# Kernel optimization log

Measured on AMD Instinct MI355X. Metric: run time of the kernel, lower is better.

## Reference

```python
import jax, jax.numpy as jnp
import numpy as np

B, S, HID = 1, 2048, 3072
NH, NKV, HD = 24, 8, 128
SCALING = 128.0 ** -0.5
SOFTCAP = 50.0
EPS = 1e-6
NEG = -1e9


def setup_inputs() -> dict:
    key = jax.random.key(0)
    ks = jax.random.split(key, 8)
    inv_freq = 1.0 / (10000.0 ** (jnp.arange(0, HD, 2, dtype=jnp.float32) / HD))
    pos = jnp.arange(S, dtype=jnp.float32)
    freqs = jnp.outer(pos, inv_freq)                      # [S, HD/2]
    emb = jnp.concatenate([freqs, freqs], axis=-1)        # [S, HD]
    cos = jnp.cos(emb)[None]                              # [B, S, HD]
    sin = jnp.sin(emb)[None]
    causal = jnp.tril(jnp.ones((S, S), dtype=bool))
    attention_mask = jnp.where(causal, 0.0, NEG).astype(jnp.float32)[None, None]  # [1,1,S,S]
    return {
        'hidden_states': jax.random.normal(ks[0], (B, S, HID), jnp.float32),
        'cos': cos,
        'sin': sin,
        'attention_mask': attention_mask,
        'wq': jax.random.normal(ks[1], (NH * HD, HID), jnp.float32) * 0.02,
        'wk': jax.random.normal(ks[2], (NKV * HD, HID), jnp.float32) * 0.02,
        'wv': jax.random.normal(ks[3], (NKV * HD, HID), jnp.float32) * 0.02,
        'wo': jax.random.normal(ks[4], (HID, NH * HD), jnp.float32) * 0.02,
        'q_norm_w': jnp.zeros((HD,), jnp.float32),
        'k_norm_w': jnp.zeros((HD,), jnp.float32),
    }


def _rms_norm(x, w, eps=EPS):
    xf = x.astype(jnp.float32)
    out = xf * jax.lax.rsqrt(jnp.mean(xf * xf, axis=-1, keepdims=True) + eps)
    return (out * (1.0 + w.astype(jnp.float32))).astype(x.dtype)


def _rotate_half(x):
    x1, x2 = jnp.split(x, 2, axis=-1)
    return jnp.concatenate([-x2, x1], axis=-1)


def reference(hidden_states, cos, sin, attention_mask, wq, wk, wv, wo, q_norm_w, k_norm_w):
    b, s, _ = hidden_states.shape
    q = jnp.einsum('bsd,ed->bse', hidden_states, wq).reshape(b, s, NH, HD).transpose(0, 2, 1, 3)
    k = jnp.einsum('bsd,ed->bse', hidden_states, wk).reshape(b, s, NKV, HD).transpose(0, 2, 1, 3)
    v = jnp.einsum('bsd,ed->bse', hidden_states, wv).reshape(b, s, NKV, HD).transpose(0, 2, 1, 3)
    q = _rms_norm(q, q_norm_w)
    k = _rms_norm(k, k_norm_w)
    c = cos[:, None]  # [B,1,S,HD]
    sn = sin[:, None]
    q = q * c + _rotate_half(q) * sn
    k = k * c + _rotate_half(k) * sn
    n_rep = NH // NKV
    k = jnp.repeat(k, n_rep, axis=1)  # [B,NH,S,HD]
    v = jnp.repeat(v, n_rep, axis=1)
    scores = jnp.einsum('bhqd,bhkd->bhqk', q, k) * SCALING
    scores = jnp.tanh(scores / SOFTCAP) * SOFTCAP
    scores = scores + attention_mask
    probs = jax.nn.softmax(scores.astype(jnp.float32), axis=-1).astype(q.dtype)
    out = jnp.einsum('bhqk,bhkd->bhqd', probs, v)
    out = out.transpose(0, 2, 1, 3).reshape(b, s, NH * HD)
    return jnp.einsum('bse,de->bsd', out, wo)
```

## Files before the change

kernel.cpp:

```cpp
#include <hip/hip_runtime.h>
#include <hip/hip_bf16.h>

#define S_LEN 2048
#define HIDV  3072
#define NHQ   24
#define NKVH  8
#define HDIM  128

typedef __bf16 bf16x8 __attribute__((ext_vector_type(8)));
typedef float  f32x4  __attribute__((ext_vector_type(4)));
typedef int    i32x4  __attribute__((ext_vector_type(4)));

__device__ __forceinline__ void gload_lds16(const void* g, void* l) {
    __builtin_amdgcn_global_load_lds((__attribute__((address_space(1))) void*)g,
                                     (__attribute__((address_space(3))) void*)l, 16, 0, 0);
}

__global__ void cast_all(const float* __restrict__ hs, const float* __restrict__ wq,
                         const float* __restrict__ wk, const float* __restrict__ wv,
                         const float* __restrict__ wo,
                         __hip_bfloat16* __restrict__ hsb, __hip_bfloat16* __restrict__ wf,
                         __hip_bfloat16* __restrict__ wob) {
    int c = blockIdx.x * blockDim.x + threadIdx.x;
    const float* src; __hip_bfloat16* dst; int off;
    if (c < 1572864)      { src = hs; dst = hsb;            off = c; }
    else if (c < 3932160) { src = wq; dst = wf;             off = c - 1572864; }
    else if (c < 4718592) { src = wk; dst = wf + 9437184;   off = c - 3932160; }
    else if (c < 5505024) { src = wv; dst = wf + 12582912;  off = c - 4718592; }
    else                  { src = wo; dst = wob;            off = c - 5505024; }
    float4 v = *(const float4*)(src + off * 4);
    union { __hip_bfloat16 h[4]; ushort4 u; } pk;
    pk.h[0] = __float2bfloat16(v.x);
    pk.h[1] = __float2bfloat16(v.y);
    pk.h[2] = __float2bfloat16(v.z);
    pk.h[3] = __float2bfloat16(v.w);
    *(ushort4*)(dst + off * 4) = pk.u;
}

template<int NF, int MODE>
__global__ __launch_bounds__(256) void gemm_tile(const __hip_bfloat16* __restrict__ A,
                                                 const __hip_bfloat16* __restrict__ B,
                                                 void* __restrict__ C0, void* __restrict__ C1,
                                                 void* __restrict__ C2)
{
    extern __shared__ __align__(16) char smem[];
    const int tid = threadIdx.x;
    const int w    = tid >> 6;
    const int lane = tid & 63;
    const int lr = lane & 15, lg = lane >> 4;
    const int wr = w >> 1, wc = w & 1;

    const int wg = ((int)blockIdx.x & 7) * 64 + ((int)blockIdx.x >> 3);
    const int bn = wg >> 4, bm = wg & 15;

    f32x4 zf = {0.f, 0.f, 0.f, 0.f};
    f32x4 acc[4][NF];
#pragma unroll
    for (int i = 0; i < 4; ++i)
#pragma unroll
        for (int j = 0; j < NF; ++j) acc[i][j] = zf;

    const char* Ab = (const char*)A + (size_t)(bm * 128) * 6144;
    const char* Bb = (const char*)B + (size_t)(bn * NF * 32) * 6144;
    const int NT = 48;

    int gaof[4], gbof[NF];
#pragma unroll
    for (int u_ = 0; u_ < 4; ++u_) {
        int u = tid + 256 * u_;
        int r_ = u >> 3, o_ = (u & 7) * 16;
        gaof[u_] = r_ * 6144 + (o_ ^ ((r_ & 7) << 4));
    }
#pragma unroll
    for (int u_ = 0; u_ < NF; ++u_) {
        int u = tid + 256 * u_;
        int r_ = u >> 3, o_ = (u & 7) * 16;
        gbof[u_] = r_ * 6144 + (o_ ^ ((r_ & 7) << 4));
    }

#define GT_STAGE(BUF, t) do {                                                       \
        const char* Abk_ = Ab + ((t) << 7);                                         \
        const char* Bbk_ = Bb + ((t) << 7);                                         \
        _Pragma("unroll")                                                           \
        for (int u_ = 0; u_ < 4; ++u_)                                              \
            gload_lds16(Abk_ + gaof[u_], smem + (BUF) * 16384 + tid * 16 + u_ * 4096); \
        _Pragma("unroll")                                                           \
        for (int u_ = 0; u_ < NF; ++u_)                                             \
            gload_lds16(Bbk_ + gbof[u_], smem + 32768 + (BUF) * (NF * 4096) + tid * 16 + u_ * 4096); \
    } while (0)

#define GT_COMPUTE(BUF) do {                                                        \
        bf16x8 af[4][2], bfr[NF][2];                                                \
        _Pragma("unroll")                                                           \
        for (int i = 0; i < 4; ++i) {                                               \
            int row = wr * 64 + i * 16 + lr;                                        \
            _Pragma("unroll")                                                       \
            for (int kk = 0; kk < 2; ++kk) {                                        \
                int cb = (kk * 64 + lg * 16) ^ ((row & 7) << 4);                    \
                af[i][kk] = *(const bf16x8*)(smem + (BUF) * 16384 + row * 128 + cb); \
            }                                                                       \
        }                                                                           \
        _Pragma("unroll")                                                           \
        for (int j = 0; j < NF; ++j) {                                              \
            int row = (wc * NF + j) * 16 + lr;                                      \
            _Pragma("unroll")                                                       \
            for (int kk = 0; kk < 2; ++kk) {                                        \
                int cb = (kk * 64 + lg * 16) ^ ((row & 7) << 4);                    \
                bfr[j][kk] = *(const bf16x8*)(smem + 32768 + (BUF) * (NF * 4096) + row * 128 + cb); \
            }                                                                       \
        }                                                                           \
        _Pragma("unroll")                                                           \
        for (int mi = 0; mi < 4; ++mi)                                              \
            _Pragma("unroll")                                                       \
            for (int ni = 0; ni < NF; ++ni)                                         \
                _Pragma("unroll")                                                   \
                for (int kk = 0; kk < 2; ++kk)                                      \
                    acc[mi][ni] = __builtin_amdgcn_mfma_f32_16x16x32_bf16(af[mi][kk], bfr[ni][kk], acc[mi][ni], 0, 0, 0); \
    } while (0)

    GT_STAGE(0, 0);
    __syncthreads();

    for (int t = 0; t < NT; t += 2) {
        GT_STAGE(1, t + 1);
        GT_COMPUTE(0);
        __syncthreads();
        if (t + 2 < NT) GT_STAGE(0, t + 2);
        GT_COMPUTE(1);
        __syncthreads();
    }
#undef GT_STAGE
#undef GT_COMPUTE

#pragma unroll
    for (int mi = 0; mi < 4; ++mi)
#pragma unroll
        for (int ni = 0; ni < NF; ++ni) {
            int row0 = bm * 128 + wr * 64 + mi * 16 + lg * 4;
            int col  = bn * NF * 32 + wc * NF * 16 + ni * 16 + lr;
            f32x4 v = acc[mi][ni];
            if (MODE == 0) {
#pragma unroll
                for (int j = 0; j < 4; ++j)
                    ((float*)C0)[(size_t)(row0 + j) * 3072 + col] = v[j];
            } else {
                if (col < 3072) {
#pragma unroll
                    for (int j = 0; j < 4; ++j)
                        ((__hip_bfloat16*)C0)[(size_t)(row0 + j) * 3072 + col] = __float2bfloat16(v[j]);
                } else if (col < 4096) {
#pragma unroll
                    for (int j = 0; j < 4; ++j)
                        ((__hip_bfloat16*)C1)[(size_t)(row0 + j) * 1024 + (col - 3072)] = __float2bfloat16(v[j]);
                } else {
                    union { __hip_bfloat16 h[4]; ushort4 u; } pk;
#pragma unroll
                    for (int j = 0; j < 4; ++j) pk.h[j] = __float2bfloat16(v[j]);
                    *(ushort4*)((__hip_bfloat16*)C2 + (size_t)(col - 4096) * 2048 + row0) = pk.u;
                }
            }
        }
}

__global__ void norm_rope_fused(const __hip_bfloat16* __restrict__ qpre,
                                const __hip_bfloat16* __restrict__ kpre,
                                __hip_bfloat16* __restrict__ qb, __hip_bfloat16* __restrict__ kb,
                                const float* __restrict__ qnw, const float* __restrict__ knw,
                                const float* __restrict__ cosp, const float* __restrict__ sinp)
{
    int gw = blockIdx.x * 4 + (threadIdx.x >> 6);
    int lane = threadIdx.x & 63;
    const __hip_bfloat16* row;
    const float* nw;
    __hip_bfloat16* outp;
    int s;
    if (gw < 49152) {
        s = gw / 24; int h = gw - s * 24;
        row  = qpre + (size_t)s * 3072 + h * HDIM;
        outp = qb   + (size_t)s * 3072 + h * HDIM;
        nw = qnw;
    } else {
        int g = gw - 49152;
        s = g >> 3; int h = g & 7;
        row  = kpre + (size_t)s * 1024 + h * HDIM;
        outp = kb + (size_t)h * 262144 + (size_t)s * 128;
        nw = knw;
    }
    float x1 = __bfloat162float(row[lane]), x2 = __bfloat162float(row[lane + 64]);
    float ss = x1 * x1 + x2 * x2;
#pragma unroll
    for (int xm = 1; xm < 64; xm <<= 1) ss += __shfl_xor(ss, xm, 64);
    float rs = rsqrtf(ss * (1.f / 128.f) + 1e-6f);
    float n1 = x1 * rs * (1.f + nw[lane]);
    float n2 = x2 * rs * (1.f + nw[lane + 64]);
    float c1 = cosp[s * HDIM + lane], c2 = cosp[s * HDIM + lane + 64];
    float s1 = sinp[s * HDIM + lane], s2 = sinp[s * HDIM + lane + 64];
    outp[lane]      = __float2bfloat16(n1 * c1 - n2 * s1);
    outp[lane + 64] = __float2bfloat16(n2 * c2 + n1 * s2);
}

__global__ __launch_bounds__(384) void attn_kernel(
    const __hip_bfloat16* __restrict__ Q,
    const __hip_bfloat16* __restrict__ Kc,
    const __hip_bfloat16* __restrict__ Vt,
    __hip_bfloat16* __restrict__ O)
{
    extern __shared__ __align__(16) char smem[];
    const int bid = blockIdx.x;
    const int kh = bid & 7;
    const int pb = bid >> 3;
    const int tid = threadIdx.x;
    const int w = tid >> 6;
    const int lane = tid & 63;
    const int lr = lane & 15, lg = lane >> 4;
    const int h = kh * 3 + (w >> 1);
    const int strip = w & 1;

    const char* kg = (const char*)(Kc + (size_t)kh * S_LEN * HDIM);
    const char* vg = (const char*)(Vt + (size_t)kh * HDIM * S_LEN);
    __hip_bfloat16* pw = (__hip_bfloat16*)(smem + 65536 + w * 2304);

    int ksrc[4], vsrc[4];
#pragma unroll
    for (int i_ = 0; i_ < 4; ++i_) {
        int base_ = (tid + 256 * i_) * 16;
        int kr_ = base_ >> 8, kc_ = base_ & 255;
        ksrc[i_] = kr_ * 256 + (kc_ ^ ((kr_ & 7) << 4));
        int vr_ = base_ >> 7, vc_ = base_ & 127;
        vsrc[i_] = vr_ * 4096 + (vc_ ^ ((vr_ & 7) << 4));
    }

#define ATT_STAGE(b, j0s) do {                                                      \
        if (tid < 256) {                                                            \
            const char* kgs_ = kg + (size_t)(j0s) * 256;                            \
            const char* vgs_ = vg + (size_t)(j0s) * 2;                              \
            _Pragma("unroll")                                                       \
            for (int i_ = 0; i_ < 4; ++i_) {                                        \
                gload_lds16(kgs_ + ksrc[i_], smem + (b) * 16384 + tid * 16 + i_ * 4096); \
                gload_lds16(vgs_ + vsrc[i_], smem + 32768 + (b) * 16384 + tid * 16 + i_ * 4096); \
            } } } while (0)

    for (int half = 0; half < 2; ++half) {
        const int hb = half ? (63 - pb) : pb;
        const int q0 = hb * 32;
        const int qrow = q0 + strip * 16;
        const int jtmax = (q0 + 31) >> 6;

        bf16x8 aq[4];
        {
            const __hip_bfloat16* qp = Q + (size_t)(qrow + lr) * HIDV + h * HDIM + lg * 8;
#pragma unroll
            for (int ks = 0; ks < 4; ++ks) aq[ks] = *(const bf16x8*)(qp + ks * 32);
        }

        f32x4 zf = {0.f, 0.f, 0.f, 0.f};
        f32x4 oacc[8];
#pragma unroll
        for (int i = 0; i < 8; ++i) oacc[i] = zf;
        float lacc[4] = {0.f, 0.f, 0.f, 0.f};

        ATT_STAGE(0, 0);
        __syncthreads();

        int buf = 0;
        for (int jt = 0; jt <= jtmax; ++jt) {
            if (jt < jtmax) ATT_STAGE(buf ^ 1, (jt + 1) * 64);

            const int j0 = jt * 64;
            const char* Kb = smem + buf * 16384;
            const char* Vb = smem + 32768 + buf * 16384;

            f32x4 sf[4];
#pragma unroll
            for (int nf = 0; nf < 4; ++nf) {
                sf[nf] = zf;
                int row = nf * 16 + lr;
#pragma unroll
                for (int ks = 0; ks < 4; ++ks) {
                    int boff = (row * 256 + ks * 64 + lg * 16) ^ ((row & 7) << 4);
                    bf16x8 bk = *(const bf16x8*)(Kb + boff);
                    sf[nf] = __builtin_amdgcn_mfma_f32_16x16x32_bf16(aq[ks], bk, sf[nf], 0, 0, 0);
                }
            }

            const bool diag = (jt == jtmax);
#pragma unroll
            for (int nf = 0; nf < 4; ++nf) {
                int jpos = j0 + nf * 16 + lr;
#pragma unroll
                for (int r = 0; r < 4; ++r) {
                    float sv = sf[nf][r];
                    float x2   = sv * sv * 3.125e-06f;
                    float poly = fmaf(x2, fmaf(x2, 0.13333333f, -0.33333333f), 1.0f);
                    float t    = sv * 0.08838834764831845f * poly;
                    float p    = __expf(t - 30.f);
                    if (diag && jpos > (qrow + lg * 4 + r)) p = 0.f;
                    lacc[r] += p;
                    pw[(lg * 4 + r) * 72 + nf * 16 + lr] = __float2bfloat16(p);
                }
            }

#pragma unroll
            for (int ks2 = 0; ks2 < 2; ++ks2) {
                bf16x8 ap = *(const bf16x8*)((const char*)pw + lr * 144 + ks2 * 64 + lg * 16);
#pragma unroll
                for (int df = 0; df < 8; ++df) {
                    int row = df * 16 + lr;
                    int boff = (row * 128 + ks2 * 64 + lg * 16) ^ ((row & 7) << 4);
                    bf16x8 bv = *(const bf16x8*)(Vb + boff);
                    oacc[df] = __builtin_amdgcn_mfma_f32_16x16x32_bf16(ap, bv, oacc[df], 0, 0, 0);
                }
            }
            __syncthreads();
            buf ^= 1;
        }

#pragma unroll
        for (int r = 0; r < 4; ++r) {
            float t = lacc[r];
#pragma unroll
            for (int xm = 1; xm < 16; xm <<= 1) t += __shfl_xor(t, xm, 64);
            float inv = __builtin_amdgcn_rcpf(t);
            size_t rowoff = (size_t)(qrow + lg * 4 + r) * HIDV + h * HDIM;
#pragma unroll
            for (int df = 0; df < 8; ++df)
                O[rowoff + df * 16 + lr] = __float2bfloat16(oacc[df][r] * inv);
        }
    }
#undef ATT_STAGE
}

extern "C" void kernel_launch(void* const* d_in, const int* in_sizes, int n_in,
                              void* d_out, int out_size, void* d_ws, size_t ws_size,
                              hipStream_t stream) {
    const float* hs   = (const float*)d_in[0];
    const float* cosp = (const float*)d_in[1];
    const float* sinp = (const float*)d_in[2];
    const float* wq  = (const float*)d_in[4];
    const float* wk  = (const float*)d_in[5];
    const float* wv  = (const float*)d_in[6];
    const float* wo  = (const float*)d_in[7];
    const float* qnw = (const float*)d_in[8];
    const float* knw = (const float*)d_in[9];
    float* out = (float*)d_out;

    char* ws = (char*)d_ws;
    __hip_bfloat16* hsb  = (__hip_bfloat16*)(ws + 0);
    __hip_bfloat16* wf   = (__hip_bfloat16*)(ws + 12582912);
    __hip_bfloat16* wob  = (__hip_bfloat16*)(ws + 44040192);
    __hip_bfloat16* qpre = (__hip_bfloat16*)(ws + 62914560);
    __hip_bfloat16* kpre = (__hip_bfloat16*)(ws + 75497472);
    __hip_bfloat16* qb   = (__hip_bfloat16*)(ws + 79691776);
    __hip_bfloat16* kb   = (__hip_bfloat16*)(ws + 92274688);
    __hip_bfloat16* vbt  = (__hip_bfloat16*)(ws + 96468992);
    __hip_bfloat16* ob   = (__hip_bfloat16*)(ws + 100663296);

    cast_all<<<30720, 256, 0, stream>>>(hs, wq, wk, wv, wo, hsb, wf, wob);

    gemm_tile<5, 1><<<512, 256, 73728, stream>>>(hsb, wf, qpre, kpre, vbt);

    norm_rope_fused<<<16384, 256, 0, stream>>>(qpre, kpre, qb, kb, qnw, knw, cosp, sinp);

    attn_kernel<<<256, 384, 79360, stream>>>(qb, kb, vbt, ob);

    gemm_tile<3, 0><<<512, 256, 57344, stream>>>(ob, wob, out, (void*)0, (void*)0);
}
```

Measured before the change: 208.6 us.

## Restructure attention to 32x32x16 MFMA with register-shuffled P and split-KV merge

Rewrites the attention inner loop to use 32x32x16 bf16 MFMA, computing S transposed (K as A operand, Q as B). The probability fragment is rebuilt in registers with cross-half lane shuffles instead of a round trip through LDS. Each pair of warps now splits one head's 64-key tile into two 32-key halves, and the partial outputs and row sums are merged through LDS at the end. The aim is to cut LDS traffic and instruction count and to shrink shared memory, at the cost of extra epilogue synchronisation and a reduction step.

Result: faster. 203.6 us (-2.4%).

```diff
diff --git a/kernel.cpp b/kernel.cpp
--- a/kernel.cpp
+++ b/kernel.cpp
@@ -9,7 +9,8 @@
 
 typedef __bf16 bf16x8 __attribute__((ext_vector_type(8)));
 typedef float  f32x4  __attribute__((ext_vector_type(4)));
-typedef int    i32x4  __attribute__((ext_vector_type(4)));
+typedef float  f32x16 __attribute__((ext_vector_type(16)));
+typedef unsigned int u32;
 
 __device__ __forceinline__ void gload_lds16(const void* g, void* l) {
     __builtin_amdgcn_global_load_lds((__attribute__((address_space(1))) void*)g,
@@ -212,20 +213,20 @@
     const int tid = threadIdx.x;
     const int w = tid >> 6;
     const int lane = tid & 63;
-    const int lr = lane & 15, lg = lane >> 4;
-    const int h = kh * 3 + (w >> 1);
-    const int strip = w & 1;
+    const int ql = lane & 31, hi = lane >> 5;
+    const int head = w >> 1;
+    const int kvh = w & 1;
+    const int h = kh * 3 + head;
 
     const char* kg = (const char*)(Kc + (size_t)kh * S_LEN * HDIM);
     const char* vg = (const char*)(Vt + (size_t)kh * HDIM * S_LEN);
-    __hip_bfloat16* pw = (__hip_bfloat16*)(smem + 65536 + w * 2304);
 
     int ksrc[4], vsrc[4];
 #pragma unroll
     for (int i_ = 0; i_ < 4; ++i_) {
         int base_ = (tid + 256 * i_) * 16;
         int kr_ = base_ >> 8, kc_ = base_ & 255;
-        ksrc[i_] = kr_ * 256 + (kc_ ^ ((kr_ & 7) << 4));
+        ksrc[i_] = kr_ * 256 + (kc_ ^ ((kr_ & 15) << 4));
         int vr_ = base_ >> 7, vc_ = base_ & 127;
         vsrc[i_] = vr_ * 4096 + (vc_ ^ ((vr_ & 7) << 4));
     }
@@ -243,21 +244,18 @@
     for (int half = 0; half < 2; ++half) {
         const int hb = half ? (63 - pb) : pb;
         const int q0 = hb * 32;
-        const int qrow = q0 + strip * 16;
+        const int qg = q0 + ql;
         const int jtmax = (q0 + 31) >> 6;
 
-        bf16x8 aq[4];
+        bf16x8 qf[8];
         {
-            const __hip_bfloat16* qp = Q + (size_t)(qrow + lr) * HIDV + h * HDIM + lg * 8;
-#pragma unroll
-            for (int ks = 0; ks < 4; ++ks) aq[ks] = *(const bf16x8*)(qp + ks * 32);
+            const char* qp = (const char*)Q + (size_t)(q0 + ql) * 6144 + h * 256 + hi * 16;
+#pragma unroll
+            for (int st = 0; st < 8; ++st) qf[st] = *(const bf16x8*)(qp + st * 32);
         }
 
-        f32x4 zf = {0.f, 0.f, 0.f, 0.f};
-        f32x4 oacc[8];
-#pragma unroll
-        for (int i = 0; i < 8; ++i) oacc[i] = zf;
-        float lacc[4] = {0.f, 0.f, 0.f, 0.f};
+        f32x16 acc_o[4] = {};
+        float lacc = 0.f;
 
         ATT_STAGE(0, 0);
         __syncthreads();
@@ -266,66 +264,114 @@
         for (int jt = 0; jt <= jtmax; ++jt) {
             if (jt < jtmax) ATT_STAGE(buf ^ 1, (jt + 1) * 64);
 
-            const int j0 = jt * 64;
             const char* Kb = smem + buf * 16384;
             const char* Vb = smem + 32768 + buf * 16384;
 
-            f32x4 sf[4];
-#pragma unroll
-            for (int nf = 0; nf < 4; ++nf) {
-                sf[nf] = zf;
-                int row = nf * 16 + lr;
-#pragma unroll
-                for (int ks = 0; ks < 4; ++ks) {
-                    int boff = (row * 256 + ks * 64 + lg * 16) ^ ((row & 7) << 4);
-                    bf16x8 bk = *(const bf16x8*)(Kb + boff);
-                    sf[nf] = __builtin_amdgcn_mfma_f32_16x16x32_bf16(aq[ks], bk, sf[nf], 0, 0, 0);
-                }
+            f32x16 sacc = {};
+            const int krow = kvh * 32 + ql;
+            const int kswz = (krow & 15) << 4;
+#pragma unroll
+            for (int st = 0; st < 8; ++st) {
+                bf16x8 kf = *(const bf16x8*)(Kb + krow * 256 + ((st * 32 + hi * 16) ^ kswz));
+                sacc = __builtin_amdgcn_mfma_f32_32x32x16_bf16(kf, qf[st], sacc, 0, 0, 0);
             }
 
             const bool diag = (jt == jtmax);
-#pragma unroll
-            for (int nf = 0; nf < 4; ++nf) {
-                int jpos = j0 + nf * 16 + lr;
-#pragma unroll
-                for (int r = 0; r < 4; ++r) {
-                    float sv = sf[nf][r];
-                    float x2   = sv * sv * 3.125e-06f;
-                    float poly = fmaf(x2, fmaf(x2, 0.13333333f, -0.33333333f), 1.0f);
-                    float t    = sv * 0.08838834764831845f * poly;
-                    float p    = __expf(t - 30.f);
-                    if (diag && jpos > (qrow + lg * 4 + r)) p = 0.f;
-                    lacc[r] += p;
-                    pw[(lg * 4 + r) * 72 + nf * 16 + lr] = __float2bfloat16(p);
-                }
+            const int kvb = jt * 64 + kvh * 32 + 4 * hi;
+            float p[16];
+#pragma unroll
+            for (int reg = 0; reg < 16; ++reg) {
+                float sv = sacc[reg];
+                float x2   = sv * sv * 3.125e-06f;
+                float poly = fmaf(x2, fmaf(x2, 0.13333333f, -0.33333333f), 1.0f);
+                float t    = sv * 0.08838834764831845f * poly;
+                float pp   = __expf(t - 30.f);
+                int kvgl = kvb + (reg & 3) + 8 * (reg >> 2);
+                if (diag && kvgl > qg) pp = 0.f;
+                lacc += pp;
+                p[reg] = pp;
             }
 
-#pragma unroll
-            for (int ks2 = 0; ks2 < 2; ++ks2) {
-                bf16x8 ap = *(const bf16x8*)((const char*)pw + lr * 144 + ks2 * 64 + lg * 16);
-#pragma unroll
-                for (int df = 0; df < 8; ++df) {
-                    int row = df * 16 + lr;
-                    int boff = (row * 128 + ks2 * 64 + lg * 16) ^ ((row & 7) << 4);
-                    bf16x8 bv = *(const bf16x8*)(Vb + boff);
-                    oacc[df] = __builtin_amdgcn_mfma_f32_16x16x32_bf16(ap, bv, oacc[df], 0, 0, 0);
+            u32 wpk[4][2];
+#pragma unroll
+            for (int o = 0; o < 4; ++o)
+#pragma unroll
+                for (int px = 0; px < 2; ++px) {
+                    union { __hip_bfloat16 hh[2]; u32 u; } cv;
+                    cv.hh[0] = __float2bfloat16(p[4 * o + 2 * px]);
+                    cv.hh[1] = __float2bfloat16(p[4 * o + 2 * px + 1]);
+                    wpk[o][px] = cv.u;
+                }
+
+            bf16x8 pfrag[2];
+#pragma unroll
+            for (int s = 0; s < 2; ++s) {
+                union { u32 u[4]; bf16x8 v; } cv;
+#pragma unroll
+                for (int px = 0; px < 2; ++px) {
+                    u32 a = wpk[2 * s][px], b = wpk[2 * s + 1][px];
+                    u32 bp = (u32)__shfl_xor((int)b, 32, 64);
+                    u32 ap = (u32)__shfl_xor((int)a, 32, 64);
+                    cv.u[px]     = hi ? bp : a;
+                    cv.u[2 + px] = hi ? b  : ap;
+                }
+                pfrag[s] = cv.v;
+            }
+
+#pragma unroll
+            for (int dt = 0; dt < 4; ++dt) {
+                const int vrow = dt * 32 + ql;
+                const int vswz = (vrow & 7) << 4;
+#pragma unroll
+                for (int s = 0; s < 2; ++s) {
+                    bf16x8 vf = *(const bf16x8*)(Vb + vrow * 128 +
+                                    ((kvh * 64 + s * 32 + hi * 16) ^ vswz));
+                    acc_o[dt] = __builtin_amdgcn_mfma_f32_32x32x16_bf16(vf, pfrag[s], acc_o[dt], 0, 0, 0);
                 }
             }
             __syncthreads();
             buf ^= 1;
         }
 
-#pragma unroll
-        for (int r = 0; r < 4; ++r) {
-            float t = lacc[r];
-#pragma unroll
-            for (int xm = 1; xm < 16; xm <<= 1) t += __shfl_xor(t, xm, 64);
-            float inv = __builtin_amdgcn_rcpf(t);
-            size_t rowoff = (size_t)(qrow + lg * 4 + r) * HIDV + h * HDIM;
-#pragma unroll
-            for (int df = 0; df < 8; ++df)
-                O[rowoff + df * 16 + lr] = __float2bfloat16(oacc[df][r] * inv);
+        float lacc2 = lacc + __shfl_xor(lacc, 32, 64);
+        const int pairbase = head * 16512;
+
+        if (kvh == 0) {
+#pragma unroll
+            for (int dt = 0; dt < 4; ++dt)
+#pragma unroll
+                for (int reg = 0; reg < 16; ++reg) {
+                    int d = dt * 32 + (reg & 3) + 8 * (reg >> 2) + 4 * hi;
+                    *(float*)(smem + pairbase + ql * 512 + ((d * 4) ^ ((ql & 15) << 5))) = acc_o[dt][reg];
+                }
+            *(float*)(smem + pairbase + 16384 + ql * 4) = lacc2;
         }
+        __syncthreads();
+        if (kvh == 1) {
+            float ltot = lacc2 + *(const float*)(smem + pairbase + 16384 + ql * 4);
+            float inv = __builtin_amdgcn_rcpf(ltot);
+#pragma unroll
+            for (int dt = 0; dt < 4; ++dt)
+#pragma unroll
+                for (int reg = 0; reg < 16; ++reg) {
+                    int d = dt * 32 + (reg & 3) + 8 * (reg >> 2) + 4 * hi;
+                    float m = acc_o[dt][reg] +
+                        *(const float*)(smem + pairbase + ql * 512 + ((d * 4) ^ ((ql & 15) << 5)));
+                    acc_o[dt][reg] = m * inv;
+                }
+            __hip_bfloat16* orow = O + (size_t)(q0 + ql) * HIDV + h * HDIM;
+#pragma unroll
+            for (int dt = 0; dt < 4; ++dt)
+#pragma unroll
+                for (int rq = 0; rq < 4; ++rq) {
+                    int d0 = dt * 32 + 8 * rq + 4 * hi;
+                    union { __hip_bfloat16 hh[4]; ushort4 u; } pk;
+#pragma unroll
+                    for (int j = 0; j < 4; ++j) pk.hh[j] = __float2bfloat16(acc_o[dt][4 * rq + j]);
+                    *(ushort4*)(orow + d0) = pk.u;
+                }
+        }
+        __syncthreads();
     }
 #undef ATT_STAGE
 }
@@ -361,7 +407,7 @@
 
     norm_rope_fused<<<16384, 256, 0, stream>>>(qpre, kpre, qb, kb, qnw, knw, cosp, sinp);
 
-    attn_kernel<<<256, 384, 79360, stream>>>(qb, kb, vbt, ob);
+    attn_kernel<<<256, 384, 65536, stream>>>(qb, kb, vbt, ob);
 
     gemm_tile<3, 0><<<512, 256, 57344, stream>>>(ob, wob, out, (void*)0, (void*)0);
 }
```

## Restructure attention to 32x32 MFMA with KV-split waves and register P

Applied to the files above, without the earlier changes.

Rewrites the attention kernel so each wave handles 64 query rows of one head against half of each 64-key tile, using 32x32x16 MFMAs with K/V as the A operand. The probability tile now stays in registers, repacked with cross-half shuffles instead of a round trip through LDS. The two KV-half partial outputs are merged through shared memory at the end. The query block grows to 64 rows with causal pairing across halves, and fully masked diagonal sub-tiles are skipped. The aim is fewer LDS round trips and higher MFMA efficiency, at the cost of more registers and an extra merge step with syncs.

After: 351.6 us. +68.5%, slower.

```diff
diff --git a/kernel.cpp b/kernel.cpp
--- a/kernel.cpp
+++ b/kernel.cpp
@@ -9,7 +9,8 @@
 
 typedef __bf16 bf16x8 __attribute__((ext_vector_type(8)));
 typedef float  f32x4  __attribute__((ext_vector_type(4)));
-typedef int    i32x4  __attribute__((ext_vector_type(4)));
+typedef float  f32x16 __attribute__((ext_vector_type(16)));
+typedef unsigned int u32;
 
 __device__ __forceinline__ void gload_lds16(const void* g, void* l) {
     __builtin_amdgcn_global_load_lds((__attribute__((address_space(1))) void*)g,
@@ -199,7 +200,7 @@
     outp[lane + 64] = __float2bfloat16(n2 * c2 + n1 * s2);
 }
 
-__global__ __launch_bounds__(384) void attn_kernel(
+__global__ __launch_bounds__(384, 2) void attn_kernel(
     const __hip_bfloat16* __restrict__ Q,
     const __hip_bfloat16* __restrict__ Kc,
     const __hip_bfloat16* __restrict__ Vt,
@@ -208,24 +209,24 @@
     extern __shared__ __align__(16) char smem[];
     const int bid = blockIdx.x;
     const int kh = bid & 7;
-    const int pb = bid >> 3;
+    const int qp = bid >> 3;
     const int tid = threadIdx.x;
     const int w = tid >> 6;
     const int lane = tid & 63;
-    const int lr = lane & 15, lg = lane >> 4;
-    const int h = kh * 3 + (w >> 1);
-    const int strip = w & 1;
+    const int ql = lane & 31, hi = lane >> 5;
+    const int head = w >> 1;
+    const int kvh = w & 1;
+    const int h = kh * 3 + head;
 
     const char* kg = (const char*)(Kc + (size_t)kh * S_LEN * HDIM);
     const char* vg = (const char*)(Vt + (size_t)kh * HDIM * S_LEN);
-    __hip_bfloat16* pw = (__hip_bfloat16*)(smem + 65536 + w * 2304);
 
     int ksrc[4], vsrc[4];
 #pragma unroll
     for (int i_ = 0; i_ < 4; ++i_) {
         int base_ = (tid + 256 * i_) * 16;
         int kr_ = base_ >> 8, kc_ = base_ & 255;
-        ksrc[i_] = kr_ * 256 + (kc_ ^ ((kr_ & 7) << 4));
+        ksrc[i_] = kr_ * 256 + (kc_ ^ ((kr_ & 15) << 4));
         int vr_ = base_ >> 7, vc_ = base_ & 127;
         vsrc[i_] = vr_ * 4096 + (vc_ ^ ((vr_ & 7) << 4));
     }
@@ -241,23 +242,22 @@
             } } } while (0)
 
     for (int half = 0; half < 2; ++half) {
-        const int hb = half ? (63 - pb) : pb;
-        const int q0 = hb * 32;
-        const int qrow = q0 + strip * 16;
-        const int jtmax = (q0 + 31) >> 6;
-
-        bf16x8 aq[4];
+        const int qb = half ? (31 - qp) : qp;
+        const int q0 = qb * 64;
+        const int jtmax = qb;
+
+        bf16x8 qf0[8], qf1[8];
         {
-            const __hip_bfloat16* qp = Q + (size_t)(qrow + lr) * HIDV + h * HDIM + lg * 8;
-#pragma unroll
-            for (int ks = 0; ks < 4; ++ks) aq[ks] = *(const bf16x8*)(qp + ks * 32);
+            const char* qp0 = (const char*)Q + (size_t)(q0 + ql) * 6144 + h * 256 + hi * 16;
+#pragma unroll
+            for (int st = 0; st < 8; ++st) {
+                qf0[st] = *(const bf16x8*)(qp0 + st * 32);
+                qf1[st] = *(const bf16x8*)(qp0 + 32 * 6144 + st * 32);
+            }
         }
 
-        f32x4 zf = {0.f, 0.f, 0.f, 0.f};
-        f32x4 oacc[8];
-#pragma unroll
-        for (int i = 0; i < 8; ++i) oacc[i] = zf;
-        float lacc[4] = {0.f, 0.f, 0.f, 0.f};
+        f32x16 acc_o0[4] = {}, acc_o1[4] = {};
+        float lacc0 = 0.f, lacc1 = 0.f;
 
         ATT_STAGE(0, 0);
         __syncthreads();
@@ -266,66 +266,124 @@
         for (int jt = 0; jt <= jtmax; ++jt) {
             if (jt < jtmax) ATT_STAGE(buf ^ 1, (jt + 1) * 64);
 
-            const int j0 = jt * 64;
             const char* Kb = smem + buf * 16384;
             const char* Vb = smem + 32768 + buf * 16384;
 
-            f32x4 sf[4];
-#pragma unroll
-            for (int nf = 0; nf < 4; ++nf) {
-                sf[nf] = zf;
-                int row = nf * 16 + lr;
-#pragma unroll
-                for (int ks = 0; ks < 4; ++ks) {
-                    int boff = (row * 256 + ks * 64 + lg * 16) ^ ((row & 7) << 4);
-                    bf16x8 bk = *(const bf16x8*)(Kb + boff);
-                    sf[nf] = __builtin_amdgcn_mfma_f32_16x16x32_bf16(aq[ks], bk, sf[nf], 0, 0, 0);
-                }
+            f32x16 sacc0 = {}, sacc1 = {};
+            const int krow = kvh * 32 + ql;
+            const int kswz = (krow & 15) << 4;
+            const bool diag = (jt == jtmax);
+            const bool skip0 = diag && (kvh == 1);
+#pragma unroll
+            for (int st = 0; st < 8; ++st) {
+                bf16x8 kf = *(const bf16x8*)(Kb + krow * 256 + ((st * 32 + hi * 16) ^ kswz));
+                if (!skip0) sacc0 = __builtin_amdgcn_mfma_f32_32x32x16_bf16(kf, qf0[st], sacc0, 0, 0, 0);
+                sacc1 = __builtin_amdgcn_mfma_f32_32x32x16_bf16(kf, qf1[st], sacc1, 0, 0, 0);
             }
 
-            const bool diag = (jt == jtmax);
-#pragma unroll
-            for (int nf = 0; nf < 4; ++nf) {
-                int jpos = j0 + nf * 16 + lr;
-#pragma unroll
-                for (int r = 0; r < 4; ++r) {
-                    float sv = sf[nf][r];
-                    float x2   = sv * sv * 3.125e-06f;
-                    float poly = fmaf(x2, fmaf(x2, 0.13333333f, -0.33333333f), 1.0f);
-                    float t    = sv * 0.08838834764831845f * poly;
-                    float p    = __expf(t - 30.f);
-                    if (diag && jpos > (qrow + lg * 4 + r)) p = 0.f;
-                    lacc[r] += p;
-                    pw[(lg * 4 + r) * 72 + nf * 16 + lr] = __float2bfloat16(p);
-                }
-            }
-
-#pragma unroll
-            for (int ks2 = 0; ks2 < 2; ++ks2) {
-                bf16x8 ap = *(const bf16x8*)((const char*)pw + lr * 144 + ks2 * 64 + lg * 16);
-#pragma unroll
-                for (int df = 0; df < 8; ++df) {
-                    int row = df * 16 + lr;
-                    int boff = (row * 128 + ks2 * 64 + lg * 16) ^ ((row & 7) << 4);
-                    bf16x8 bv = *(const bf16x8*)(Vb + boff);
-                    oacc[df] = __builtin_amdgcn_mfma_f32_16x16x32_bf16(ap, bv, oacc[df], 0, 0, 0);
+            const int kvb = jt * 64 + kvh * 32 + 4 * hi;
+
+#define SMAX_SET(SACC, LACC, PFRAG, QG, MASKED) do {                                \
+            float p_[16];                                                           \
+            _Pragma("unroll")                                                       \
+            for (int reg = 0; reg < 16; ++reg) {                                    \
+                float sv = (SACC)[reg];                                             \
+                float x2_   = sv * sv * 3.125e-06f;                                 \
+                float poly_ = fmaf(x2_, fmaf(x2_, 0.13333333f, -0.33333333f), 1.0f);\
+                float t_    = sv * 0.08838834764831845f * poly_;                    \
+                float pp_   = __expf(t_ - 30.f);                                    \
+                if ((MASKED) && (kvb + (reg & 3) + 8 * (reg >> 2)) > (QG)) pp_ = 0.f; \
+                (LACC) += pp_;                                                      \
+                p_[reg] = pp_;                                                      \
+            }                                                                       \
+            u32 wpk_[4][2];                                                         \
+            _Pragma("unroll")                                                       \
+            for (int o = 0; o < 4; ++o)                                             \
+                _Pragma("unroll")                                                   \
+                for (int px = 0; px < 2; ++px) {                                    \
+                    union { __hip_bfloat16 hh[2]; u32 u; } cv_;                     \
+                    cv_.hh[0] = __float2bfloat16(p_[4 * o + 2 * px]);               \
+                    cv_.hh[1] = __float2bfloat16(p_[4 * o + 2 * px + 1]);           \
+                    wpk_[o][px] = cv_.u;                                            \
+                }                                                                   \
+            _Pragma("unroll")                                                       \
+            for (int s = 0; s < 2; ++s) {                                           \
+                union { u32 u[4]; bf16x8 v; } cv_;                                  \
+                _Pragma("unroll")                                                   \
+                for (int px = 0; px < 2; ++px) {                                    \
+                    u32 a_ = wpk_[2 * s][px], b_ = wpk_[2 * s + 1][px];             \
+                    u32 send_ = hi ? a_ : b_;                                       \
+                    u32 recv_ = (u32)__shfl_xor((int)send_, 32, 64);                \
+                    cv_.u[px]     = hi ? recv_ : a_;                                \
+                    cv_.u[2 + px] = hi ? b_    : recv_;                             \
+                }                                                                   \
+                (PFRAG)[s] = cv_.v;                                                 \
+            } } while (0)
+
+            bf16x8 pfrag0[2], pfrag1[2];
+            if (!skip0) SMAX_SET(sacc0, lacc0, pfrag0, q0 + ql,      diag && (kvh == 0));
+            SMAX_SET(sacc1, lacc1, pfrag1, q0 + 32 + ql, diag && (kvh == 1));
+#undef SMAX_SET
+
+#pragma unroll
+            for (int dt = 0; dt < 4; ++dt) {
+                const int vrow = dt * 32 + ql;
+                const int vswz = (vrow & 7) << 4;
+#pragma unroll
+                for (int s = 0; s < 2; ++s) {
+                    bf16x8 vf = *(const bf16x8*)(Vb + vrow * 128 +
+                                    ((kvh * 64 + s * 32 + hi * 16) ^ vswz));
+                    if (!skip0) acc_o0[dt] = __builtin_amdgcn_mfma_f32_32x32x16_bf16(vf, pfrag0[s], acc_o0[dt], 0, 0, 0);
+                    acc_o1[dt] = __builtin_amdgcn_mfma_f32_32x32x16_bf16(vf, pfrag1[s], acc_o1[dt], 0, 0, 0);
                 }
             }
             __syncthreads();
             buf ^= 1;
         }
 
-#pragma unroll
-        for (int r = 0; r < 4; ++r) {
-            float t = lacc[r];
-#pragma unroll
-            for (int xm = 1; xm < 16; xm <<= 1) t += __shfl_xor(t, xm, 64);
-            float inv = __builtin_amdgcn_rcpf(t);
-            size_t rowoff = (size_t)(qrow + lg * 4 + r) * HIDV + h * HDIM;
-#pragma unroll
-            for (int df = 0; df < 8; ++df)
-                O[rowoff + df * 16 + lr] = __float2bfloat16(oacc[df][r] * inv);
-        }
+        const int pairbase = head * 16512;
+#define MERGE_STORE(ACCO, LACC, SROW) do {                                          \
+        float l2_ = (LACC) + __shfl_xor((LACC), 32, 64);                            \
+        if (kvh == 0) {                                                             \
+            _Pragma("unroll")                                                       \
+            for (int dt = 0; dt < 4; ++dt)                                          \
+                _Pragma("unroll")                                                   \
+                for (int reg = 0; reg < 16; ++reg) {                                \
+                    int d_ = dt * 32 + (reg & 3) + 8 * (reg >> 2) + 4 * hi;         \
+                    *(float*)(smem + pairbase + ql * 512 + ((d_ * 4) ^ ((ql & 15) << 5))) = (ACCO)[dt][reg]; \
+                }                                                                   \
+            *(float*)(smem + pairbase + 16384 + ql * 4) = l2_;                      \
+        }                                                                           \
+        __syncthreads();                                                            \
+        if (kvh == 1) {                                                             \
+            float lt_ = l2_ + *(const float*)(smem + pairbase + 16384 + ql * 4);    \
+            float inv_ = __builtin_amdgcn_rcpf(lt_);                                \
+            _Pragma("unroll")                                                       \
+            for (int dt = 0; dt < 4; ++dt)                                          \
+                _Pragma("unroll")                                                   \
+                for (int reg = 0; reg < 16; ++reg) {                                \
+                    int d_ = dt * 32 + (reg & 3) + 8 * (reg >> 2) + 4 * hi;         \
+                    float m_ = (ACCO)[dt][reg] +                                    \
+                        *(const float*)(smem + pairbase + ql * 512 + ((d_ * 4) ^ ((ql & 15) << 5))); \
+                    (ACCO)[dt][reg] = m_ * inv_;                                    \
+                }                                                                   \
+            __hip_bfloat16* orow_ = O + (size_t)(SROW) * HIDV + h * HDIM;           \
+            _Pragma("unroll")                                                       \
+            for (int dt = 0; dt < 4; ++dt)                                          \
+                _Pragma("unroll")                                                   \
+                for (int rq = 0; rq < 4; ++rq) {                                    \
+                    int d0_ = dt * 32 + 8 * rq + 4 * hi;                            \
+                    union { __hip_bfloat16 hh[4]; ushort4 u; } pk_;                 \
+                    _Pragma("unroll")                                               \
+                    for (int j = 0; j < 4; ++j) pk_.hh[j] = __float2bfloat16((ACCO)[dt][4 * rq + j]); \
+                    *(ushort4*)(orow_ + d0_) = pk_.u;                               \
+                }                                                                   \
+        }                                                                           \
+        __syncthreads(); } while (0)
+
+        MERGE_STORE(acc_o0, lacc0, q0 + ql);
+        MERGE_STORE(acc_o1, lacc1, q0 + 32 + ql);
+#undef MERGE_STORE
     }
 #undef ATT_STAGE
 }
@@ -361,7 +419,7 @@
 
     norm_rope_fused<<<16384, 256, 0, stream>>>(qpre, kpre, qb, kb, qnw, knw, cosp, sinp);
 
-    attn_kernel<<<256, 384, 79360, stream>>>(qb, kb, vbt, ob);
+    attn_kernel<<<256, 384, 65536, stream>>>(qb, kb, vbt, ob);
 
     gemm_tile<3, 0><<<512, 256, 57344, stream>>>(ob, wob, out, (void*)0, (void*)0);
 }
```
